# Kernel optimization log

Hardware: AMD Instinct MI355X
Metric: run time of the kernel (lower is better)

Reference implementation:

```python
import jax, jax.numpy as jnp
import numpy as np


def setup_inputs() -> dict:
    key = jax.random.key(0)
    k1, k2 = jax.random.split(key)
    B, C, H, W = 32, 256, 64, 64
    data = jax.random.normal(k1, (B, C, H, W), dtype=jnp.float32)
    offset = jax.random.normal(k2, (B, 2, H, W), dtype=jnp.float32)
    trans_std = jnp.float32(0.005)  # learned scalar Parameter
    return {"data": data, "offset": offset, "trans_std": trans_std}


def reference(data, offset, trans_std):
    """Offset-driven bilinear interpolation sampling + global average pooling.

    data:   [B, C, H, W]
    offset: [B, 2, H, W]  (dy, dx) displacement field, scaled by trans_std
    Returns pooled features [B, C].
    """
    B, C, H, W = data.shape
    ts = jnp.clip(trans_std, 0.001, 0.01)  # forward clamps trans_std to [0.001, 0.01]

    # sampling coordinates: base grid + scaled offsets (offsets normalized by H/W)
    ii = jnp.arange(H, dtype=data.dtype)[:, None]   # [H,1]
    jj = jnp.arange(W, dtype=data.dtype)[None, :]   # [1,W]
    y = jnp.clip(ii + ts * offset[:, 0] * H, 0.0, H - 1)  # [B,H,W]
    x = jnp.clip(jj + ts * offset[:, 1] * W, 0.0, W - 1)  # [B,H,W]

    y0 = jnp.clip(jnp.floor(y).astype(jnp.int32), 0, H - 2)
    x0 = jnp.clip(jnp.floor(x).astype(jnp.int32), 0, W - 2)
    y1 = y0 + 1
    x1 = x0 + 1
    wy = y - y0.astype(data.dtype)  # [B,H,W] in [0,1]
    wx = x - x0.astype(data.dtype)

    def sample_one(d, yy0, yy1, xx0, xx1):
        # d: [C,H,W]; index maps: [H,W] -> gathered [C,H,W]
        v00 = d[:, yy0, xx0]
        v01 = d[:, yy0, xx1]
        v10 = d[:, yy1, xx0]
        v11 = d[:, yy1, xx1]
        return v00, v01, v10, v11

    v00, v01, v10, v11 = jax.vmap(sample_one)(data, y0, y1, x0, x1)  # each [B,C,H,W]

    wy_ = wy[:, None]  # broadcast over channels -> [B,1,H,W]
    wx_ = wx[:, None]
    sampled = ((1 - wy_) * (1 - wx_) * v00 + (1 - wy_) * wx_ * v01
               + wy_ * (1 - wx_) * v10 + wy_ * wx_ * v11)  # [B,C,H,W]

    # pooling: global average over spatial locations -> [B,C]
    return jnp.mean(sampled, axis=(2, 3))
```

## Files before the change

kernel.cpp:

```cpp
#include <hip/hip_runtime.h>

#define BATCH 32
#define CHAN  256
#define HGT   64
#define WID   64
#define HW    4096

typedef float v4f __attribute__((ext_vector_type(4)));

__global__ __launch_bounds__(256) void weight_map_kernel(
        const float* __restrict__ offset,
        const float* __restrict__ ts_ptr,
        float* __restrict__ A)
{
    const int b   = blockIdx.x;
    const int tid = threadIdx.x;

    __shared__ float acc[HW];
    for (int k = tid; k < HW; k += 256) acc[k] = 0.0f;
    __syncthreads();

    float ts = ts_ptr[0];
    ts = fminf(fmaxf(ts, 0.001f), 0.01f);

    const float* off_y = offset + (size_t)b * 2 * HW;
    const float* off_x = off_y + HW;

    #pragma unroll 4
    for (int p = tid; p < HW; p += 256) {
        const int i = p >> 6;
        const int j = p & 63;
        const float dy = off_y[p];
        const float dx = off_x[p];
        float y = fminf(fmaxf((float)i + ts * dy * 64.0f, 0.0f), 63.0f);
        float x = fminf(fmaxf((float)j + ts * dx * 64.0f, 0.0f), 63.0f);
        int y0 = (int)floorf(y); y0 = min(max(y0, 0), HGT - 2);
        int x0 = (int)floorf(x); x0 = min(max(x0, 0), WID - 2);
        const float wy = y - (float)y0;
        const float wx = x - (float)x0;
        const int base = (y0 << 6) + x0;
        atomicAdd(&acc[base],           (1.0f - wy) * (1.0f - wx));
        atomicAdd(&acc[base + 1],       (1.0f - wy) * wx);
        atomicAdd(&acc[base + WID],     wy * (1.0f - wx));
        atomicAdd(&acc[base + WID + 1], wy * wx);
    }
    __syncthreads();

    float* Ab = A + (size_t)b * HW;
    const float s = 1.0f / (float)HW;
    for (int k = tid; k < HW; k += 256) Ab[k] = acc[k] * s;
}

__global__ __launch_bounds__(256, 8) void dot_kernel(
        const float* __restrict__ data,
        const float* __restrict__ A,
        float* __restrict__ out)
{
    const int wave = (blockIdx.x << 2) + (threadIdx.x >> 6);
    const int lane = threadIdx.x & 63;
    const int b    = wave >> 8;

    const float* plane = data + (size_t)wave * HW;
    const float* Ab    = A    + (size_t)b    * HW;

    float sum = 0.0f;
    #pragma unroll
    for (int it = 0; it < 4; ++it) {
        const int i0 = ((it * 4 + 0) * 64 + lane) * 4;
        const int i1 = ((it * 4 + 1) * 64 + lane) * 4;
        const int i2 = ((it * 4 + 2) * 64 + lane) * 4;
        const int i3 = ((it * 4 + 3) * 64 + lane) * 4;

        const v4f d0 = __builtin_nontemporal_load(
                           reinterpret_cast<const v4f*>(plane + i0));
        const v4f d1 = __builtin_nontemporal_load(
                           reinterpret_cast<const v4f*>(plane + i1));
        const v4f d2 = __builtin_nontemporal_load(
                           reinterpret_cast<const v4f*>(plane + i2));
        const v4f d3 = __builtin_nontemporal_load(
                           reinterpret_cast<const v4f*>(plane + i3));
        const v4f a0 = *reinterpret_cast<const v4f*>(Ab + i0);
        const v4f a1 = *reinterpret_cast<const v4f*>(Ab + i1);
        const v4f a2 = *reinterpret_cast<const v4f*>(Ab + i2);
        const v4f a3 = *reinterpret_cast<const v4f*>(Ab + i3);

        sum = fmaf(a0.x, d0.x, sum); sum = fmaf(a0.y, d0.y, sum);
        sum = fmaf(a0.z, d0.z, sum); sum = fmaf(a0.w, d0.w, sum);
        sum = fmaf(a1.x, d1.x, sum); sum = fmaf(a1.y, d1.y, sum);
        sum = fmaf(a1.z, d1.z, sum); sum = fmaf(a1.w, d1.w, sum);
        sum = fmaf(a2.x, d2.x, sum); sum = fmaf(a2.y, d2.y, sum);
        sum = fmaf(a2.z, d2.z, sum); sum = fmaf(a2.w, d2.w, sum);
        sum = fmaf(a3.x, d3.x, sum); sum = fmaf(a3.y, d3.y, sum);
        sum = fmaf(a3.z, d3.z, sum); sum = fmaf(a3.w, d3.w, sum);
    }

    #pragma unroll
    for (int off = 32; off > 0; off >>= 1)
        sum += __shfl_down(sum, off, 64);

    if (lane == 0) out[wave] = sum;
}

extern "C" void kernel_launch(void* const* d_in, const int* in_sizes, int n_in,
                              void* d_out, int out_size, void* d_ws, size_t ws_size,
                              hipStream_t stream) {
    const float* data   = (const float*)d_in[0];
    const float* offset = (const float*)d_in[1];
    const float* ts     = (const float*)d_in[2];

    float* A   = (float*)d_ws;
    float* out = (float*)d_out;

    weight_map_kernel<<<BATCH, 256, 0, stream>>>(offset, ts, A);
    dot_kernel<<<(BATCH * CHAN) / 4, 256, 0, stream>>>(data, A, out);
}
```

Baseline: 219.6 us.

## Fuse weight-map construction and channel dot product into one kernel

Merges the two launches into one kernel: each 1024-thread block rebuilds the per-batch bilinear weight map in shared memory, then 16 waves each dot it against one channel plane. This drops the second launch, the global workspace round trip for the weight map, and the serial dependency where only 32 blocks built the maps. In exchange the weight map is recomputed 16 times per batch (extra offset reads and LDS atomics), and the nontemporal load hint on data is removed.

```diff
diff --git a/kernel.cpp b/kernel.cpp
--- a/kernel.cpp
+++ b/kernel.cpp
@@ -5,19 +5,25 @@
 #define HGT   64
 #define WID   64
 #define HW    4096
+#define CPB   16
 
-typedef float v4f __attribute__((ext_vector_type(4)));
-
-__global__ __launch_bounds__(256) void weight_map_kernel(
+__global__ __launch_bounds__(1024, 8) void fused_bilinear_pool(
+        const float* __restrict__ data,
         const float* __restrict__ offset,
         const float* __restrict__ ts_ptr,
-        float* __restrict__ A)
+        float* __restrict__ out)
 {
-    const int b   = blockIdx.x;
+    const int blk = blockIdx.x;
+    const int b   = blk >> 4;
+    const int g   = blk & 15;
     const int tid = threadIdx.x;
 
     __shared__ float acc[HW];
-    for (int k = tid; k < HW; k += 256) acc[k] = 0.0f;
+
+    acc[tid]        = 0.0f;
+    acc[tid + 1024] = 0.0f;
+    acc[tid + 2048] = 0.0f;
+    acc[tid + 3072] = 0.0f;
     __syncthreads();
 
     float ts = ts_ptr[0];
@@ -26,8 +32,9 @@
     const float* off_y = offset + (size_t)b * 2 * HW;
     const float* off_x = off_y + HW;
 
-    #pragma unroll 4
-    for (int p = tid; p < HW; p += 256) {
+    #pragma unroll
+    for (int it = 0; it < 4; ++it) {
+        const int p = tid + it * 1024;
         const int i = p >> 6;
         const int j = p & 63;
         const float dy = off_y[p];
@@ -46,43 +53,27 @@
     }
     __syncthreads();
 
-    float* Ab = A + (size_t)b * HW;
-    const float s = 1.0f / (float)HW;
-    for (int k = tid; k < HW; k += 256) Ab[k] = acc[k] * s;
-}
+    const int w    = tid >> 6;
+    const int lane = tid & 63;
 
-__global__ __launch_bounds__(256, 8) void dot_kernel(
-        const float* __restrict__ data,
-        const float* __restrict__ A,
-        float* __restrict__ out)
-{
-    const int wave = (blockIdx.x << 2) + (threadIdx.x >> 6);
-    const int lane = threadIdx.x & 63;
-    const int b    = wave >> 8;
-
-    const float* plane = data + (size_t)wave * HW;
-    const float* Ab    = A    + (size_t)b    * HW;
+    const float* plane = data + ((size_t)(b * CHAN + g * CPB + w)) * HW;
 
     float sum = 0.0f;
     #pragma unroll
-    for (int it = 0; it < 4; ++it) {
-        const int i0 = ((it * 4 + 0) * 64 + lane) * 4;
-        const int i1 = ((it * 4 + 1) * 64 + lane) * 4;
-        const int i2 = ((it * 4 + 2) * 64 + lane) * 4;
-        const int i3 = ((it * 4 + 3) * 64 + lane) * 4;
+    for (int k = 0; k < 4; ++k) {
+        const int i0 = k * 1024 + 0   + lane * 4;
+        const int i1 = k * 1024 + 256 + lane * 4;
+        const int i2 = k * 1024 + 512 + lane * 4;
+        const int i3 = k * 1024 + 768 + lane * 4;
 
-        const v4f d0 = __builtin_nontemporal_load(
-                           reinterpret_cast<const v4f*>(plane + i0));
-        const v4f d1 = __builtin_nontemporal_load(
-                           reinterpret_cast<const v4f*>(plane + i1));
-        const v4f d2 = __builtin_nontemporal_load(
-                           reinterpret_cast<const v4f*>(plane + i2));
-        const v4f d3 = __builtin_nontemporal_load(
-                           reinterpret_cast<const v4f*>(plane + i3));
-        const v4f a0 = *reinterpret_cast<const v4f*>(Ab + i0);
-        const v4f a1 = *reinterpret_cast<const v4f*>(Ab + i1);
-        const v4f a2 = *reinterpret_cast<const v4f*>(Ab + i2);
-        const v4f a3 = *reinterpret_cast<const v4f*>(Ab + i3);
+        const float4 d0 = *reinterpret_cast<const float4*>(plane + i0);
+        const float4 d1 = *reinterpret_cast<const float4*>(plane + i1);
+        const float4 d2 = *reinterpret_cast<const float4*>(plane + i2);
+        const float4 d3 = *reinterpret_cast<const float4*>(plane + i3);
+        const float4 a0 = *reinterpret_cast<const float4*>(acc + i0);
+        const float4 a1 = *reinterpret_cast<const float4*>(acc + i1);
+        const float4 a2 = *reinterpret_cast<const float4*>(acc + i2);
+        const float4 a3 = *reinterpret_cast<const float4*>(acc + i3);
 
         sum = fmaf(a0.x, d0.x, sum); sum = fmaf(a0.y, d0.y, sum);
         sum = fmaf(a0.z, d0.z, sum); sum = fmaf(a0.w, d0.w, sum);
@@ -98,7 +89,8 @@
     for (int off = 32; off > 0; off >>= 1)
         sum += __shfl_down(sum, off, 64);
 
-    if (lane == 0) out[wave] = sum;
+    if (lane == 0)
+        out[(b << 8) + g * CPB + w] = sum * (1.0f / (float)HW);
 }
 
 extern "C" void kernel_launch(void* const* d_in, const int* in_sizes, int n_in,
@@ -108,9 +100,8 @@
     const float* offset = (const float*)d_in[1];
     const float* ts     = (const float*)d_in[2];
 
-    float* A   = (float*)d_ws;
     float* out = (float*)d_out;
+    (void)d_ws; (void)ws_size;
 
-    weight_map_kernel<<<BATCH, 256, 0, stream>>>(offset, ts, A);
-    dot_kernel<<<(BATCH * CHAN) / 4, 256, 0, stream>>>(data, A, out);
+    fused_bilinear_pool<<<BATCH * CPB, 1024, 0, stream>>>(data, offset, ts, out);
 }
```

Result: no change. 220.5 us (+0.4%).
